# Kernel tuning notes

Hardware: AMD Instinct MI355X
Metric: run time of the kernel (lower is better)

The kernel has to match this reference:

```python
import jax, jax.numpy as jnp
import numpy as np

B, S, D_IN, D_OUT, H = 2, 2048, 1024, 1024, 16
HD = D_OUT // H


def setup_inputs() -> dict:
    key = jax.random.key(0)
    ks = jax.random.split(key, 6)
    s = 0.02
    return {
        "X": jax.random.normal(ks[0], (B, S, D_IN), dtype=jnp.float32),
        "Wq": jax.random.normal(ks[1], (D_OUT, D_IN), dtype=jnp.float32) * s,
        "Wk": jax.random.normal(ks[2], (D_OUT, D_IN), dtype=jnp.float32) * s,
        "Wv": jax.random.normal(ks[3], (D_OUT, D_IN), dtype=jnp.float32) * s,
        "Wo": jax.random.normal(ks[4], (D_OUT, D_OUT), dtype=jnp.float32) * s,
        "bo": jax.random.normal(ks[5], (D_OUT,), dtype=jnp.float32) * s,
    }


def reference(X, Wq, Wk, Wv, Wo, bo):
    b, n, _ = X.shape
    # torch Linear: y = x @ W^T
    Q = (X @ Wq.T).reshape(b, n, H, HD).transpose(0, 2, 1, 3)  # [b,h,s,hd]
    K = (X @ Wk.T).reshape(b, n, H, HD).transpose(0, 2, 1, 3)
    V = (X @ Wv.T).reshape(b, n, H, HD).transpose(0, 2, 1, 3)
    S_ = jnp.einsum('bhqd,bhkd->bhqk', Q, K)  # [b,h,s,s]
    causal = jnp.triu(jnp.ones((n, n), dtype=bool), k=1)
    S_ = jnp.where(causal, -jnp.inf, S_)
    W = jax.nn.softmax(S_ / jnp.sqrt(jnp.float32(HD)), axis=-1)
    Z = jnp.einsum('bhqk,bhkd->bhqd', W, V)
    Z = Z.transpose(0, 2, 1, 3).reshape(b, n, D_OUT)
    return Z @ Wo.T + bo
```

## Files before the change

kernel.cpp:

```cpp
#include <hip/hip_runtime.h>
#include <stdint.h>

typedef __bf16 bf16x8 __attribute__((ext_vector_type(8)));
typedef float  f32x4  __attribute__((ext_vector_type(4)));

#define S_   2048
#define DM   1024
#define QSCALE 0.18033688011112042f

__device__ __forceinline__ unsigned short f2b(float f) {
    uint32_t u = __builtin_bit_cast(uint32_t, f);
    u += 0x7fffu + ((u >> 16) & 1u);
    return (unsigned short)(u >> 16);
}

__device__ __forceinline__ uint32_t pack2bf(float a, float b) {
    uint32_t ua = __builtin_bit_cast(uint32_t, a) + 0x8000u;
    uint32_t ub = __builtin_bit_cast(uint32_t, b) + 0x8000u;
    return __builtin_amdgcn_perm(ub, ua, 0x07060302);
}

__device__ __forceinline__ void glds16(const void* g, void* l) {
    __builtin_amdgcn_global_load_lds(
        (const __attribute__((address_space(1))) void*)g,
        (__attribute__((address_space(3))) void*)l, 16, 0, 0);
}

__global__ void cvt_all(const float* __restrict__ X,
                        const float* __restrict__ Wq, const float* __restrict__ Wk,
                        const float* __restrict__ Wv,
                        unsigned short* __restrict__ Xb, unsigned short* __restrict__ Wb)
{
    size_t i = ((size_t)blockIdx.x * 256 + threadIdx.x) * 4;
    const float* src;
    unsigned short* dst;
    size_t off;
    if (i < (size_t)4194304) { src = X; dst = Xb; off = i; }
    else {
        size_t j = i - 4194304;
        int sel = (int)(j >> 20);
        off = j & 1048575;
        src = (sel == 0) ? Wq : (sel == 1) ? Wk : Wv;
        dst = Wb + (size_t)sel * 1048576;
    }
    float4 v = *(const float4*)&src[off];
    uint2 o;
    o.x = pack2bf(v.x, v.y);
    o.y = pack2bf(v.z, v.w);
    *(uint2*)&dst[off] = o;
}

__global__ void cvt_wo(const float* __restrict__ Wo, unsigned short* __restrict__ Wob)
{
    size_t i = ((size_t)blockIdx.x * 256 + threadIdx.x) * 4;
    float4 v = *(const float4*)&Wo[i];
    uint2 o;
    o.x = pack2bf(v.x, v.y);
    o.y = pack2bf(v.z, v.w);
    *(uint2*)&Wob[i] = o;
}

__global__ __launch_bounds__(256, 2)
void qkv_gemm(const unsigned short* __restrict__ Xb,
              const unsigned short* __restrict__ Wqb,
              const unsigned short* __restrict__ Wkb,
              const unsigned short* __restrict__ Wvb,
              unsigned short* __restrict__ Qo, unsigned short* __restrict__ Ko,
              unsigned short* __restrict__ Vto)
{
    __shared__ unsigned short Ash[128 * 32];
    __shared__ unsigned short Bsh[128 * 32];

    const int t = threadIdx.x;
    const int lane = t & 63, w = t >> 6;
    const int lcol = lane & 15, quad = lane >> 4;
    const int z = blockIdx.z;
    const int rowBase = ((z == 2) ? blockIdx.x : blockIdx.y) * 128;
    const int colBase = ((z == 2) ? blockIdx.y : blockIdx.x) * 128;
    const unsigned short* aPtr = (z == 2) ? Wvb : Xb;
    const unsigned short* bPtr = (z == 0) ? Wqb : (z == 1) ? Wkb : Xb;
    const int wr = (w >> 1) * 64, wc = (w & 1) * 64;

    f32x4 acc[4][4];
    #pragma unroll
    for (int i = 0; i < 4; ++i)
        #pragma unroll
        for (int j = 0; j < 4; ++j) acc[i][j] = (f32x4){0.f,0.f,0.f,0.f};

    for (int k0 = 0; k0 < DM; k0 += 32) {
        __syncthreads();
        #pragma unroll
        for (int p = 0; p < 2; ++p) {
            int ci = p * 256 + t;
            glds16(&aPtr[(size_t)(rowBase + (ci >> 2)) * DM + k0 + (ci & 3) * 8], &Ash[ci * 8]);
        }
        #pragma unroll
        for (int p = 0; p < 2; ++p) {
            int ci = p * 256 + t;
            glds16(&bPtr[(size_t)(colBase + (ci >> 2)) * DM + k0 + (ci & 3) * 8], &Bsh[ci * 8]);
        }
        __syncthreads();
        bf16x8 af[4], bfr[4];
        #pragma unroll
        for (int i = 0; i < 4; ++i) af[i]  = *(const bf16x8*)&Ash[(wr + i*16 + lcol)*32 + quad*8];
        #pragma unroll
        for (int i = 0; i < 4; ++i) bfr[i] = *(const bf16x8*)&Bsh[(wc + i*16 + lcol)*32 + quad*8];
        #pragma unroll
        for (int i = 0; i < 4; ++i)
            #pragma unroll
            for (int j = 0; j < 4; ++j)
                acc[i][j] = __builtin_amdgcn_mfma_f32_16x16x32_bf16(af[i], bfr[j], acc[i][j], 0, 0, 0);
    }

    unsigned short* Cm = (z == 0) ? Qo : (z == 1) ? Ko : Vto;
    const int ld = (z == 2) ? (S_ * 2) : DM;
    const float sc = (z == 0) ? QSCALE : 1.0f;
    #pragma unroll
    for (int i = 0; i < 4; ++i)
        #pragma unroll
        for (int j = 0; j < 4; ++j)
            #pragma unroll
            for (int r = 0; r < 4; ++r) {
                int row = rowBase + wr + i*16 + quad*4 + r;
                int col = colBase + wc + j*16 + lcol;
                Cm[(size_t)row * ld + col] = f2b(acc[i][j][r] * sc);
            }
}

__global__ __launch_bounds__(512, 4)
void attn_kernel(const unsigned short* __restrict__ Q,
                 const unsigned short* __restrict__ K,
                 const unsigned short* __restrict__ Vt,
                 unsigned short* __restrict__ Z)
{
    __shared__ unsigned short Ks[2][64 * 72];
    __shared__ unsigned short Vts[2][64 * 72];
    __shared__ unsigned short Ps[128 * 72];

    const int t = threadIdx.x;
    const int lane = t & 63, w = t >> 6;
    const int lcol = lane & 15, quad = lane >> 4;

    const int bh = blockIdx.x;
    const int b = bh >> 4, h = bh & 15;
    const int y = blockIdx.y;
    const int tile = (y < 8) ? (15 - y) : (y - 8);
    const int q0 = tile * 128;
    const int nchunk = 2 * tile + 2;

    const unsigned short* Qg = Q + (size_t)(b * S_ + q0) * DM + h * 64;
    const unsigned short* Kg = K + (size_t)(b * S_) * DM + h * 64;
    const unsigned short* Vg = Vt + (size_t)(h * 64) * (S_ * 2) + b * S_;

    bf16x8 qf[2];
    #pragma unroll
    for (int kd = 0; kd < 2; ++kd)
        qf[kd] = *(const bf16x8*)&Qg[(size_t)(w*16 + lcol) * DM + kd*32 + quad*8];

    bool mk[4];
    #pragma unroll
    for (int r = 0; r < 4; ++r) mk[r] = (quad*4 + r) > lcol;

    float lpart = 0.f;
    f32x4 o[4];
    #pragma unroll
    for (int nd = 0; nd < 4; ++nd) o[nd] = (f32x4){0.f,0.f,0.f,0.f};

    const int sr = t >> 3, sch = t & 7;

    {
        uint4 k0 = *(const uint4*)&Kg[(size_t)sr * DM + sch * 8];
        uint4 v0 = *(const uint4*)&Vg[(size_t)sr * (S_ * 2) + sch * 8];
        *(uint4*)&Ks[0][sr * 72 + sch * 8] = k0;
        *(uint4*)&Vts[0][sr * 72 + sch * 8] = v0;
    }
    __syncthreads();

    for (int c = 0; c < nchunk; ++c) {
        const int cur = c & 1;
        const bool pf = (c + 1 < nchunk);
        uint4 kn, vn;
        if (pf) {
            const int kc1 = (c + 1) * 64;
            kn = *(const uint4*)&Kg[(size_t)(kc1 + sr) * DM + sch * 8];
            vn = *(const uint4*)&Vg[(size_t)sr * (S_ * 2) + kc1 + sch * 8];
        }

        const unsigned short* Kc = Ks[cur];
        const unsigned short* Vc = Vts[cur];

        const int m = tile * 8 + w - c * 4;
        const int nkmax = (m >= 3) ? 4 : (m + 1);
        const int kdmax = (nkmax + 1) >> 1;

        #pragma unroll
        for (int nk = 0; nk < 4; ++nk) {
            if (nk < nkmax) {
                f32x4 s = (f32x4){0.f,0.f,0.f,0.f};
                bf16x8 ak0 = *(const bf16x8*)&Kc[(nk*16 + lcol)*72 + quad*8];
                s = __builtin_amdgcn_mfma_f32_16x16x32_bf16(ak0, qf[0], s, 0, 0, 0);
                bf16x8 ak1 = *(const bf16x8*)&Kc[(nk*16 + lcol)*72 + 32 + quad*8];
                s = __builtin_amdgcn_mfma_f32_16x16x32_bf16(ak1, qf[1], s, 0, 0, 0);
                float p0 = __builtin_amdgcn_exp2f(s[0]);
                float p1 = __builtin_amdgcn_exp2f(s[1]);
                float p2 = __builtin_amdgcn_exp2f(s[2]);
                float p3 = __builtin_amdgcn_exp2f(s[3]);
                if (nk == m) {
                    p0 = mk[0] ? 0.f : p0;
                    p1 = mk[1] ? 0.f : p1;
                    p2 = mk[2] ? 0.f : p2;
                    p3 = mk[3] ? 0.f : p3;
                }
                lpart += (p0 + p1) + (p2 + p3);
                uint2 pk;
                pk.x = pack2bf(p0, p1);
                pk.y = pack2bf(p2, p3);
                *(uint2*)&Ps[(w*16 + lcol) * 72 + nk*16 + quad*4] = pk;
            } else if (nk < 2*kdmax) {
                *(uint2*)&Ps[(w*16 + lcol) * 72 + nk*16 + quad*4] = (uint2){0u, 0u};
            }
        }

        #pragma unroll
        for (int kd2 = 0; kd2 < 2; ++kd2) {
            if (kd2 < kdmax) {
                bf16x8 ap = *(const bf16x8*)&Ps[(w*16 + lcol) * 72 + kd2*32 + quad*8];
                #pragma unroll
                for (int nd = 0; nd < 4; ++nd) {
                    bf16x8 bv = *(const bf16x8*)&Vc[(nd*16 + lcol) * 72 + kd2*32 + quad*8];
                    o[nd] = __builtin_amdgcn_mfma_f32_16x16x32_bf16(ap, bv, o[nd], 0, 0, 0);
                }
            }
        }

        if (pf) {
            *(uint4*)&Ks[cur ^ 1][sr * 72 + sch * 8] = kn;
            *(uint4*)&Vts[cur ^ 1][sr * 72 + sch * 8] = vn;
        }
        __syncthreads();
    }

    lpart += __shfl_xor(lpart, 16);
    lpart += __shfl_xor(lpart, 32);
    float linv = 1.0f / lpart;
    #pragma unroll
    for (int r = 0; r < 4; ++r) {
        float lr = __shfl(linv, quad*4 + r);
        unsigned short* Zr = Z + (size_t)(b*S_ + q0 + w*16 + quad*4 + r) * DM + h*64;
        #pragma unroll
        for (int nd = 0; nd < 4; ++nd)
            Zr[nd*16 + lcol] = f2b(o[nd][r] * lr);
    }
}

__global__ __launch_bounds__(256, 4)
void out_gemm(const unsigned short* __restrict__ A,
              const unsigned short* __restrict__ Wob, const float* __restrict__ bo,
              float* __restrict__ Out)
{
    __shared__ unsigned short Ash[64 * 32];
    __shared__ unsigned short Bsh[128 * 32];

    const int t = threadIdx.x;
    const int lane = t & 63, w = t >> 6;
    const int lcol = lane & 15, quad = lane >> 4;
    const int rowBase = blockIdx.y * 64;
    const int colBase = blockIdx.x * 128;
    const int wr = (w >> 1) * 32, wc = (w & 1) * 64;

    f32x4 acc[2][4];
    #pragma unroll
    for (int i = 0; i < 2; ++i)
        #pragma unroll
        for (int j = 0; j < 4; ++j) acc[i][j] = (f32x4){0.f,0.f,0.f,0.f};

    for (int k0 = 0; k0 < DM; k0 += 32) {
        __syncthreads();
        glds16(&A[(size_t)(rowBase + (t >> 2)) * DM + k0 + (t & 3) * 8], &Ash[t * 8]);
        #pragma unroll
        for (int p = 0; p < 2; ++p) {
            int ci = p * 256 + t;
            glds16(&Wob[(size_t)(colBase + (ci >> 2)) * DM + k0 + (ci & 3) * 8], &Bsh[ci * 8]);
        }
        __syncthreads();
        bf16x8 af[2], bfr[4];
        #pragma unroll
        for (int i = 0; i < 2; ++i) af[i]  = *(const bf16x8*)&Ash[(wr + i*16 + lcol)*32 + quad*8];
        #pragma unroll
        for (int j = 0; j < 4; ++j) bfr[j] = *(const bf16x8*)&Bsh[(wc + j*16 + lcol)*32 + quad*8];
        #pragma unroll
        for (int i = 0; i < 2; ++i)
            #pragma unroll
            for (int j = 0; j < 4; ++j)
                acc[i][j] = __builtin_amdgcn_mfma_f32_16x16x32_bf16(af[i], bfr[j], acc[i][j], 0, 0, 0);
    }

    float bb[4];
    #pragma unroll
    for (int j = 0; j < 4; ++j) bb[j] = bo[colBase + wc + j*16 + lcol];

    #pragma unroll
    for (int i = 0; i < 2; ++i)
        #pragma unroll
        for (int j = 0; j < 4; ++j)
            #pragma unroll
            for (int r = 0; r < 4; ++r) {
                int row = rowBase + wr + i*16 + quad*4 + r;
                int col = colBase + wc + j*16 + lcol;
                Out[(size_t)row * DM + col] = acc[i][j][r] + bb[j];
            }
}

extern "C" void kernel_launch(void* const* d_in, const int* in_sizes, int n_in,
                              void* d_out, int out_size, void* d_ws, size_t ws_size,
                              hipStream_t stream) {
    const float* X  = (const float*)d_in[0];
    const float* Wq = (const float*)d_in[1];
    const float* Wk = (const float*)d_in[2];
    const float* Wv = (const float*)d_in[3];
    const float* Wo = (const float*)d_in[4];
    const float* bo = (const float*)d_in[5];
    float* out = (float*)d_out;

    unsigned short* Xb  = (unsigned short*)d_ws;
    unsigned short* Qw  = Xb + (size_t)4096 * 1024;
    unsigned short* Kw  = Qw + (size_t)4096 * 1024;
    unsigned short* Vtw = Kw + (size_t)4096 * 1024;
    unsigned short* Zb  = Xb;
    unsigned short* Wob = Qw;
    unsigned short* Wb  = (unsigned short*)d_out;

    cvt_all<<<dim3(7168), 256, 0, stream>>>(X, Wq, Wk, Wv, Xb, Wb);
    qkv_gemm<<<dim3(8, 32, 3), 256, 0, stream>>>(Xb, Wb, Wb + (size_t)1048576,
                                                 Wb + (size_t)2097152, Qw, Kw, Vtw);
    attn_kernel<<<dim3(32, 16), 512, 0, stream>>>(Qw, Kw, Vtw, Zb);
    cvt_wo<<<dim3(1024), 256, 0, stream>>>(Wo, Wob);
    out_gemm<<<dim3(8, 64), 256, 0, stream>>>(Zb, Wob, bo, out);
}
```

Baseline: 185.3 us.

## Split attention key chunk across warp pairs, keep P in registers via shuffles

Each warp now handles 32 query rows and one half of each 64-key chunk instead of 16 rows over the full chunk, so every K fragment read from LDS feeds two query tiles. The P tile no longer round-trips through shared memory: lane-exchange shuffles rebuild the MFMA A operand in registers, and the V read index is permuted to match. Partial outputs and row sums from the two key halves are combined through shared memory at the end. The cost is more registers per thread, an extra barrier and a reduction step, and half the warps sit idle during the final normalisation and store.

```diff
diff --git a/kernel.cpp b/kernel.cpp
--- a/kernel.cpp
+++ b/kernel.cpp
@@ -3,6 +3,7 @@
 
 typedef __bf16 bf16x8 __attribute__((ext_vector_type(8)));
 typedef float  f32x4  __attribute__((ext_vector_type(4)));
+typedef unsigned int u32x4 __attribute__((ext_vector_type(4)));
 
 #define S_   2048
 #define DM   1024
@@ -133,13 +134,12 @@
                  const unsigned short* __restrict__ Vt,
                  unsigned short* __restrict__ Z)
 {
-    __shared__ unsigned short Ks[2][64 * 72];
-    __shared__ unsigned short Vts[2][64 * 72];
-    __shared__ unsigned short Ps[128 * 72];
+    __shared__ __align__(16) unsigned short SH[18432];
 
     const int t = threadIdx.x;
     const int lane = t & 63, w = t >> 6;
     const int lcol = lane & 15, quad = lane >> 4;
+    const int kh = w & 1, wq = w >> 1;
 
     const int bh = blockIdx.x;
     const int b = bh >> 4, h = bh & 15;
@@ -152,29 +152,37 @@
     const unsigned short* Kg = K + (size_t)(b * S_) * DM + h * 64;
     const unsigned short* Vg = Vt + (size_t)(h * 64) * (S_ * 2) + b * S_;
 
-    bf16x8 qf[2];
-    #pragma unroll
-    for (int kd = 0; kd < 2; ++kd)
-        qf[kd] = *(const bf16x8*)&Qg[(size_t)(w*16 + lcol) * DM + kd*32 + quad*8];
+    bf16x8 qf[2][2];
+    #pragma unroll
+    for (int qi = 0; qi < 2; ++qi)
+        #pragma unroll
+        for (int kd = 0; kd < 2; ++kd)
+            qf[qi][kd] = *(const bf16x8*)&Qg[(size_t)(wq*32 + qi*16 + lcol) * DM + kd*32 + quad*8];
 
     bool mk[4];
     #pragma unroll
     for (int r = 0; r < 4; ++r) mk[r] = (quad*4 + r) > lcol;
 
-    float lpart = 0.f;
-    f32x4 o[4];
-    #pragma unroll
-    for (int nd = 0; nd < 4; ++nd) o[nd] = (f32x4){0.f,0.f,0.f,0.f};
+    float lp[2] = {0.f, 0.f};
+    f32x4 o[2][4];
+    #pragma unroll
+    for (int qi = 0; qi < 2; ++qi)
+        #pragma unroll
+        for (int nd = 0; nd < 4; ++nd) o[qi][nd] = (f32x4){0.f,0.f,0.f,0.f};
 
     const int sr = t >> 3, sch = t & 7;
 
     {
         uint4 k0 = *(const uint4*)&Kg[(size_t)sr * DM + sch * 8];
         uint4 v0 = *(const uint4*)&Vg[(size_t)sr * (S_ * 2) + sch * 8];
-        *(uint4*)&Ks[0][sr * 72 + sch * 8] = k0;
-        *(uint4*)&Vts[0][sr * 72 + sch * 8] = v0;
+        *(uint4*)&SH[sr * 72 + sch * 8] = k0;
+        *(uint4*)&SH[9216 + sr * 72 + sch * 8] = v0;
     }
     __syncthreads();
+
+    const int Qb0 = tile * 8 + wq * 2;
+    const int gq = ((quad & 1) << 1) | (quad >> 1);
+    const bool qodd = (quad & 1) != 0;
 
     for (int c = 0; c < nchunk; ++c) {
         const int cur = c & 1;
@@ -185,71 +193,120 @@
             kn = *(const uint4*)&Kg[(size_t)(kc1 + sr) * DM + sch * 8];
             vn = *(const uint4*)&Vg[(size_t)sr * (S_ * 2) + kc1 + sch * 8];
         }
-
-        const unsigned short* Kc = Ks[cur];
-        const unsigned short* Vc = Vts[cur];
-
-        const int m = tile * 8 + w - c * 4;
-        const int nkmax = (m >= 3) ? 4 : (m + 1);
-        const int kdmax = (nkmax + 1) >> 1;
-
-        #pragma unroll
-        for (int nk = 0; nk < 4; ++nk) {
-            if (nk < nkmax) {
-                f32x4 s = (f32x4){0.f,0.f,0.f,0.f};
-                bf16x8 ak0 = *(const bf16x8*)&Kc[(nk*16 + lcol)*72 + quad*8];
-                s = __builtin_amdgcn_mfma_f32_16x16x32_bf16(ak0, qf[0], s, 0, 0, 0);
-                bf16x8 ak1 = *(const bf16x8*)&Kc[(nk*16 + lcol)*72 + 32 + quad*8];
-                s = __builtin_amdgcn_mfma_f32_16x16x32_bf16(ak1, qf[1], s, 0, 0, 0);
-                float p0 = __builtin_amdgcn_exp2f(s[0]);
-                float p1 = __builtin_amdgcn_exp2f(s[1]);
-                float p2 = __builtin_amdgcn_exp2f(s[2]);
-                float p3 = __builtin_amdgcn_exp2f(s[3]);
-                if (nk == m) {
-                    p0 = mk[0] ? 0.f : p0;
-                    p1 = mk[1] ? 0.f : p1;
-                    p2 = mk[2] ? 0.f : p2;
-                    p3 = mk[3] ? 0.f : p3;
+        const unsigned short* Kc = &SH[cur * 4608];
+        const unsigned short* Vc = &SH[9216 + cur * 4608];
+
+        const int Kb0 = c * 4 + kh * 2;
+        if (Kb0 <= Qb0 + 1) {
+            uint32_t pw[2][2][2];
+            #pragma unroll
+            for (int nk = 0; nk < 2; ++nk) {
+                const int Kb = Kb0 + nk;
+                if (Kb <= Qb0 + 1) {
+                    bf16x8 ak0 = *(const bf16x8*)&Kc[(kh*32 + nk*16 + lcol)*72 + quad*8];
+                    bf16x8 ak1 = *(const bf16x8*)&Kc[(kh*32 + nk*16 + lcol)*72 + 32 + quad*8];
+                    #pragma unroll
+                    for (int qi = 0; qi < 2; ++qi) {
+                        if (Kb <= Qb0 + qi) {
+                            f32x4 s = (f32x4){0.f,0.f,0.f,0.f};
+                            s = __builtin_amdgcn_mfma_f32_16x16x32_bf16(ak0, qf[qi][0], s, 0, 0, 0);
+                            s = __builtin_amdgcn_mfma_f32_16x16x32_bf16(ak1, qf[qi][1], s, 0, 0, 0);
+                            float p0 = __builtin_amdgcn_exp2f(s[0]);
+                            float p1 = __builtin_amdgcn_exp2f(s[1]);
+                            float p2 = __builtin_amdgcn_exp2f(s[2]);
+                            float p3 = __builtin_amdgcn_exp2f(s[3]);
+                            if (Kb == Qb0 + qi) {
+                                p0 = mk[0] ? 0.f : p0;
+                                p1 = mk[1] ? 0.f : p1;
+                                p2 = mk[2] ? 0.f : p2;
+                                p3 = mk[3] ? 0.f : p3;
+                            }
+                            lp[qi] += (p0 + p1) + (p2 + p3);
+                            pw[qi][nk][0] = pack2bf(p0, p1);
+                            pw[qi][nk][1] = pack2bf(p2, p3);
+                        } else {
+                            pw[qi][nk][0] = 0u;
+                            pw[qi][nk][1] = 0u;
+                        }
+                    }
+                } else {
+                    #pragma unroll
+                    for (int qi = 0; qi < 2; ++qi) {
+                        pw[qi][nk][0] = 0u;
+                        pw[qi][nk][1] = 0u;
+                    }
                 }
-                lpart += (p0 + p1) + (p2 + p3);
-                uint2 pk;
-                pk.x = pack2bf(p0, p1);
-                pk.y = pack2bf(p2, p3);
-                *(uint2*)&Ps[(w*16 + lcol) * 72 + nk*16 + quad*4] = pk;
-            } else if (nk < 2*kdmax) {
-                *(uint2*)&Ps[(w*16 + lcol) * 72 + nk*16 + quad*4] = (uint2){0u, 0u};
-            }
-        }
-
-        #pragma unroll
-        for (int kd2 = 0; kd2 < 2; ++kd2) {
-            if (kd2 < kdmax) {
-                bf16x8 ap = *(const bf16x8*)&Ps[(w*16 + lcol) * 72 + kd2*32 + quad*8];
+            }
+
+            bf16x8 ap[2];
+            #pragma unroll
+            for (int qi = 0; qi < 2; ++qi) {
+                uint32_t a0 = pw[qi][0][0], a1 = pw[qi][0][1];
+                uint32_t b0 = pw[qi][1][0], b1 = pw[qi][1][1];
+                uint32_t xa0 = (uint32_t)__shfl_xor((int)a0, 16);
+                uint32_t xa1 = (uint32_t)__shfl_xor((int)a1, 16);
+                uint32_t xb0 = (uint32_t)__shfl_xor((int)b0, 16);
+                uint32_t xb1 = (uint32_t)__shfl_xor((int)b1, 16);
+                u32x4 apw;
+                apw[0] = qodd ? xb0 : a0;
+                apw[1] = qodd ? xb1 : a1;
+                apw[2] = qodd ? b0 : xa0;
+                apw[3] = qodd ? b1 : xa1;
+                ap[qi] = __builtin_bit_cast(bf16x8, apw);
+            }
+
+            #pragma unroll
+            for (int nd = 0; nd < 4; ++nd) {
+                bf16x8 bv = *(const bf16x8*)&Vc[(nd*16 + lcol)*72 + kh*32 + gq*8];
                 #pragma unroll
-                for (int nd = 0; nd < 4; ++nd) {
-                    bf16x8 bv = *(const bf16x8*)&Vc[(nd*16 + lcol) * 72 + kd2*32 + quad*8];
-                    o[nd] = __builtin_amdgcn_mfma_f32_16x16x32_bf16(ap, bv, o[nd], 0, 0, 0);
-                }
+                for (int qi = 0; qi < 2; ++qi)
+                    o[qi][nd] = __builtin_amdgcn_mfma_f32_16x16x32_bf16(ap[qi], bv, o[qi][nd], 0, 0, 0);
             }
         }
 
         if (pf) {
-            *(uint4*)&Ks[cur ^ 1][sr * 72 + sch * 8] = kn;
-            *(uint4*)&Vts[cur ^ 1][sr * 72 + sch * 8] = vn;
-        }
-        __syncthreads();
-    }
-
-    lpart += __shfl_xor(lpart, 16);
-    lpart += __shfl_xor(lpart, 32);
-    float linv = 1.0f / lpart;
-    #pragma unroll
-    for (int r = 0; r < 4; ++r) {
-        float lr = __shfl(linv, quad*4 + r);
-        unsigned short* Zr = Z + (size_t)(b*S_ + q0 + w*16 + quad*4 + r) * DM + h*64;
-        #pragma unroll
-        for (int nd = 0; nd < 4; ++nd)
-            Zr[nd*16 + lcol] = f2b(o[nd][r] * lr);
+            *(uint4*)&SH[(cur ^ 1) * 4608 + sr * 72 + sch * 8] = kn;
+            *(uint4*)&SH[9216 + (cur ^ 1) * 4608 + sr * 72 + sch * 8] = vn;
+        }
+        __syncthreads();
+    }
+
+    #pragma unroll
+    for (int qi = 0; qi < 2; ++qi) {
+        lp[qi] += __shfl_xor(lp[qi], 16);
+        lp[qi] += __shfl_xor(lp[qi], 32);
+    }
+    float* red = (float*)SH;
+    float* my = red + (wq * 64 + lane) * 36;
+    if (kh == 1) {
+        #pragma unroll
+        for (int qi = 0; qi < 2; ++qi)
+            #pragma unroll
+            for (int nd = 0; nd < 4; ++nd)
+                *(f32x4*)&my[qi*16 + nd*4] = o[qi][nd];
+        my[32] = lp[0];
+        my[33] = lp[1];
+    }
+    __syncthreads();
+    if (kh == 0) {
+        #pragma unroll
+        for (int qi = 0; qi < 2; ++qi)
+            #pragma unroll
+            for (int nd = 0; nd < 4; ++nd)
+                o[qi][nd] += *(const f32x4*)&my[qi*16 + nd*4];
+        float linv[2];
+        linv[0] = 1.0f / (lp[0] + my[32]);
+        linv[1] = 1.0f / (lp[1] + my[33]);
+        #pragma unroll
+        for (int qi = 0; qi < 2; ++qi)
+            #pragma unroll
+            for (int r = 0; r < 4; ++r) {
+                float lr = __shfl(linv[qi], quad*4 + r);
+                unsigned short* Zr = Z + (size_t)(b*S_ + q0 + wq*32 + qi*16 + quad*4 + r) * DM + h*64;
+                #pragma unroll
+                for (int nd = 0; nd < 4; ++nd)
+                    Zr[nd*16 + lcol] = f2b(o[qi][nd][r] * lr);
+            }
     }
 }
 
```

Result: faster. 179.1 us (-3.3%).
